# Kernel optimization log

Hardware: AMD Instinct MI355X
Metric: run time of the kernel (lower is better)

Reference implementation:

```python
import jax, jax.numpy as jnp
import numpy as np

N_NODES = 50000
N_EDGES = 800000
IN_DIM = 128
HID = 64
N_LAYERS = 4  # num_layers=5 in source -> 4 GINConv layers
BN_EPS = 1e-5


def setup_inputs() -> dict:
    key = jax.random.key(0)
    ks = jax.random.split(key, 16)
    h = jax.random.normal(ks[0], (N_NODES, IN_DIM), dtype=jnp.float32)
    src = jax.random.randint(ks[1], (N_EDGES,), 0, N_NODES, dtype=jnp.int32)
    dst = jax.random.randint(ks[2], (N_EDGES,), 0, N_NODES, dtype=jnp.int32)
    s = 0.05
    # layer 0 params (IN_DIM -> HID -> HID)
    W1_0 = jax.random.normal(ks[3], (IN_DIM, HID), dtype=jnp.float32) * s
    b1_0 = jnp.zeros((HID,), jnp.float32)
    W2_0 = jax.random.normal(ks[4], (HID, HID), dtype=jnp.float32) * s
    b2_0 = jnp.zeros((HID,), jnp.float32)
    g_0 = jnp.ones((HID,), jnp.float32)
    be_0 = jnp.zeros((HID,), jnp.float32)
    # layers 1..3 params stacked (HID -> HID -> HID)
    W1s = jax.random.normal(ks[5], (N_LAYERS - 1, HID, HID), dtype=jnp.float32) * s
    b1s = jnp.zeros((N_LAYERS - 1, HID), jnp.float32)
    W2s = jax.random.normal(ks[6], (N_LAYERS - 1, HID, HID), dtype=jnp.float32) * s
    b2s = jnp.zeros((N_LAYERS - 1, HID), jnp.float32)
    gs = jnp.ones((N_LAYERS - 1, HID), jnp.float32)
    bes = jnp.zeros((N_LAYERS - 1, HID), jnp.float32)
    return dict(h=h, src=src, dst=dst,
                W1_0=W1_0, b1_0=b1_0, W2_0=W2_0, b2_0=b2_0, g_0=g_0, be_0=be_0,
                W1s=W1s, b1s=b1s, W2s=W2s, b2s=b2s, gs=gs, bes=bes)


def _gin_layer(h, src, dst, W1, b1, W2, b2, gamma, beta):
    # GINConv (eps=0, sum aggregation): z = h + sum_{j->i} h_j
    agg = jax.ops.segment_sum(h[src], dst, num_segments=N_NODES)  # [N, d]
    z = h + agg
    # MLP: Linear -> ReLU -> Linear
    z = jax.nn.relu(z @ W1 + b1) @ W2 + b2
    # BatchNorm1d (training mode: batch statistics over nodes)
    mean = jnp.mean(z, axis=0)
    var = jnp.var(z, axis=0)
    z = (z - mean) * jax.lax.rsqrt(var + BN_EPS) * gamma + beta
    return jax.nn.relu(z)


def reference(h, src, dst, W1_0, b1_0, W2_0, b2_0, g_0, be_0,
              W1s, b1s, W2s, b2s, gs, bes):
    h = _gin_layer(h, src, dst, W1_0, b1_0, W2_0, b2_0, g_0, be_0)
    for i in range(N_LAYERS - 1):
        h = _gin_layer(h, src, dst, W1s[i], b1s[i], W2s[i], b2s[i], gs[i], bes[i])
    return h
```

## Files before the change

kernel.cpp:

```cpp
#include <hip/hip_runtime.h>
#include <hip/hip_bf16.h>

static constexpr int NN = 50000;
static constexpr int NE = 800000;
static constexpr float BN_EPS = 1e-5f;

static constexpr int NB  = 128;
static constexpr int NPB = 391;
static constexpr int CAP = 8192;
static constexpr int CHUNK = 2048;
static constexpr int SRNG = 12500;

__device__ __forceinline__ float bflo(unsigned u) { return __uint_as_float(u << 16); }
__device__ __forceinline__ float bfhi(unsigned u) { return __uint_as_float(u & 0xffff0000u); }
__device__ __forceinline__ unsigned short f2bf(float f) {
    unsigned u = __float_as_uint(f);
    unsigned r = (u + 0x7fffu + ((u >> 16) & 1u)) >> 16;
    return (unsigned short)r;
}

__global__ __launch_bounds__(256) void zero_kernel(int* __restrict__ ptr, int n)
{
    int i = blockIdx.x * 256 + threadIdx.x;
    if (i < n) ptr[i] = 0;
}

__global__ __launch_bounds__(256) void binA_kernel(
    const int* __restrict__ src, const int* __restrict__ dst,
    int* __restrict__ gcount, unsigned* __restrict__ tmp)
{
    __shared__ unsigned stage[CHUNK];
    __shared__ int hist[NB], base[NB], gpos[NB];

    const int t = threadIdx.x;
    const int cb = blockIdx.x * CHUNK;
    const int total = min(CHUNK, NE - cb);

    if (t < NB) hist[t] = 0;
    __syncthreads();

    int mb[8], mslot[8];
    unsigned mv[8];
    #pragma unroll
    for (int k = 0; k < 8; ++k) {
        int e = cb + k * 256 + t;
        mb[k] = -1;
        if (e < NE) {
            int s = src[e];
            int d = dst[e];
            int b = d / NPB;
            mb[k] = b;
            mv[k] = ((unsigned)d << 16) | (unsigned)s;
            mslot[k] = atomicAdd(&hist[b], 1);
        }
    }
    __syncthreads();

    if (t < NB) base[t] = hist[t];
    __syncthreads();
    for (int ofs = 1; ofs < NB; ofs <<= 1) {
        int v = (t >= ofs && t < NB) ? base[t - ofs] : 0;
        __syncthreads();
        if (t < NB) base[t] += v;
        __syncthreads();
    }
    if (t < NB && hist[t] > 0)
        gpos[t] = t * CAP + atomicAdd(&gcount[t], hist[t]);
    __syncthreads();

    #pragma unroll
    for (int k = 0; k < 8; ++k) {
        if (mb[k] >= 0) {
            int b = mb[k];
            stage[(base[b] - hist[b]) + mslot[k]] = mv[k];
        }
    }
    __syncthreads();

    for (int i = t; i < total; i += 256) {
        unsigned v = stage[i];
        int b = (int)(v >> 16) / NPB;
        int pos = gpos[b] + (i - (base[b] - hist[b]));
        tmp[pos] = v;
    }
}

__global__ __launch_bounds__(256) void binB_kernel(
    const unsigned* __restrict__ tmp, const int* __restrict__ gcount,
    int* __restrict__ off, int* __restrict__ eidx)
{
    __shared__ int gb[NB];
    __shared__ int hist4[NPB * 4];
    __shared__ int hs[512];
    __shared__ int cur4[NPB * 4];
    __shared__ int base_s;

    const int t = threadIdx.x;
    const int b = blockIdx.x;
    const int n0 = b * NPB;
    const int n1 = min(n0 + NPB, NN);
    const int nnodes = n1 - n0;
    const int cnt = gcount[b];

    if (t < NB) gb[t] = gcount[t];
    for (int i = t; i < NPB * 4; i += 256) hist4[i] = 0;
    __syncthreads();
    for (int ofs = 1; ofs < NB; ofs <<= 1) {
        int v = (t >= ofs && t < NB) ? gb[t - ofs] : 0;
        __syncthreads();
        if (t < NB) gb[t] += v;
        __syncthreads();
    }
    if (t == 0) base_s = (b == 0) ? 0 : gb[b - 1];
    __syncthreads();
    const int base = base_s;

    const unsigned* tb = tmp + (size_t)b * CAP;
    for (int i = t; i < cnt; i += 256) {
        unsigned v = tb[i];
        int d = (int)(v >> 16);
        int s = (int)(v & 0xffffu);
        atomicAdd(&hist4[(d - n0) * 4 + s / SRNG], 1);
    }
    __syncthreads();
    {
        int n = t;
        hs[t] = (n < NPB) ? (hist4[n * 4] + hist4[n * 4 + 1] +
                             hist4[n * 4 + 2] + hist4[n * 4 + 3]) : 0;
        n = t + 256;
        hs[t + 256] = (n < NPB) ? (hist4[n * 4] + hist4[n * 4 + 1] +
                                   hist4[n * 4 + 2] + hist4[n * 4 + 3]) : 0;
    }
    __syncthreads();
    for (int ofs = 1; ofs < 512; ofs <<= 1) {
        int a0 = (t >= ofs) ? hs[t - ofs] : 0;
        int a1 = hs[t + 256 - ofs];
        __syncthreads();
        hs[t] += a0;
        hs[t + 256] += a1;
        __syncthreads();
    }
    for (int n = t; n < nnodes; n += 256) {
        int h0 = hist4[n * 4], h1 = hist4[n * 4 + 1], h2 = hist4[n * 4 + 2];
        int tot = h0 + h1 + h2 + hist4[n * 4 + 3];
        int c = base + hs[n] - tot;
        off[n0 + n] = c;
        cur4[n * 4 + 0] = c; c += h0;
        cur4[n * 4 + 1] = c; c += h1;
        cur4[n * 4 + 2] = c; c += h2;
        cur4[n * 4 + 3] = c;
    }
    if (b == NB - 1 && t == 0) off[NN] = base + cnt;
    __syncthreads();
    for (int i = t; i < cnt; i += 256) {
        unsigned v = tb[i];
        int d = (int)(v >> 16);
        int s = (int)(v & 0xffffu);
        int pos = atomicAdd(&cur4[(d - n0) * 4 + s / SRNG], 1);
        eidx[pos] = s;
    }
}

template<int D, bool NORM>
__global__ __launch_bounds__(256) void proj_kernel(
    const void* __restrict__ hin_, const float* __restrict__ W1,
    const float* __restrict__ gsum, const float* __restrict__ gsq,
    const float* __restrict__ gamma, const float* __restrict__ beta,
    unsigned short* __restrict__ p)
{
    constexpr int RPB = 128;
    __shared__ float XsT[64][132];
    __shared__ float Ws[64][64];
    __shared__ float scs[64], shs[64];

    const int t = threadIdx.x;
    const int rowbase = blockIdx.x * RPB;

    if (NORM) {
        if (t < 64) {
            const float invn = 1.f / (float)NN;
            float mean = gsum[t] * invn;
            float var  = gsq[t] * invn - mean * mean;
            float sc   = gamma[t] * rsqrtf(var + BN_EPS);
            scs[t] = sc;
            shs[t] = beta[t] - mean * sc;
        }
        __syncthreads();
    }

    const int tc = t & 7;
    const int tr = t >> 3;
    const int c0 = tc * 8;
    const int r0 = tr * 4;

    float acc[4][8];
    #pragma unroll
    for (int i = 0; i < 4; ++i)
        #pragma unroll
        for (int j = 0; j < 8; ++j) acc[i][j] = 0.f;

    for (int kc = 0; kc < D; kc += 64) {
        if (kc) __syncthreads();
        {
            const float4* wg = reinterpret_cast<const float4*>(W1 + (size_t)kc * 64);
            float4* wl = reinterpret_cast<float4*>(&Ws[0][0]);
            for (int i = t; i < 64 * 16; i += 256) wl[i] = wg[i];
        }
        if constexpr (NORM) {
            const uint4* hb = reinterpret_cast<const uint4*>(hin_);
            int rr = t & 31, q = t >> 5;
            for (int i = 0; i < RPB; i += 32) {
                int r = i + rr;
                int gr = rowbase + r;
                uint4 v = make_uint4(0u, 0u, 0u, 0u);
                if (gr < NN) v = hb[gr * 8 + q];
                int c = q * 8;
                float f0 = bflo(v.x), f1 = bfhi(v.x), f2 = bflo(v.y), f3 = bfhi(v.y);
                float f4 = bflo(v.z), f5 = bfhi(v.z), f6 = bflo(v.w), f7 = bfhi(v.w);
                XsT[c + 0][r] = fmaxf(f0 * scs[c + 0] + shs[c + 0], 0.f);
                XsT[c + 1][r] = fmaxf(f1 * scs[c + 1] + shs[c + 1], 0.f);
                XsT[c + 2][r] = fmaxf(f2 * scs[c + 2] + shs[c + 2], 0.f);
                XsT[c + 3][r] = fmaxf(f3 * scs[c + 3] + shs[c + 3], 0.f);
                XsT[c + 4][r] = fmaxf(f4 * scs[c + 4] + shs[c + 4], 0.f);
                XsT[c + 5][r] = fmaxf(f5 * scs[c + 5] + shs[c + 5], 0.f);
                XsT[c + 6][r] = fmaxf(f6 * scs[c + 6] + shs[c + 6], 0.f);
                XsT[c + 7][r] = fmaxf(f7 * scs[c + 7] + shs[c + 7], 0.f);
            }
        } else {
            const float* hin = reinterpret_cast<const float*>(hin_);
            int rr = t & 15, q = t >> 4;
            for (int i = 0; i < RPB; i += 16) {
                int r = i + rr;
                int gr = rowbase + r;
                float4 v = make_float4(0.f, 0.f, 0.f, 0.f);
                if (gr < NN)
                    v = reinterpret_cast<const float4*>(hin + (size_t)gr * D + kc)[q];
                XsT[q * 4 + 0][r] = v.x;
                XsT[q * 4 + 1][r] = v.y;
                XsT[q * 4 + 2][r] = v.z;
                XsT[q * 4 + 3][r] = v.w;
            }
        }
        __syncthreads();

        for (int k = 0; k < 64; ++k) {
            float4 xa = *reinterpret_cast<const float4*>(&XsT[k][r0]);
            float4 wa = *reinterpret_cast<const float4*>(&Ws[k][c0]);
            float4 wb = *reinterpret_cast<const float4*>(&Ws[k][c0 + 4]);
            float x[4] = { xa.x, xa.y, xa.z, xa.w };
            float w[8] = { wa.x, wa.y, wa.z, wa.w, wb.x, wb.y, wb.z, wb.w };
            #pragma unroll
            for (int i = 0; i < 4; ++i)
                #pragma unroll
                for (int j = 0; j < 8; ++j) acc[i][j] += x[i] * w[j];
        }
    }

    #pragma unroll
    for (int i = 0; i < 4; ++i) {
        int gr = rowbase + r0 + i;
        if (gr < NN) {
            uint4 u;
            u.x = (unsigned)f2bf(acc[i][0]) | ((unsigned)f2bf(acc[i][1]) << 16);
            u.y = (unsigned)f2bf(acc[i][2]) | ((unsigned)f2bf(acc[i][3]) << 16);
            u.z = (unsigned)f2bf(acc[i][4]) | ((unsigned)f2bf(acc[i][5]) << 16);
            u.w = (unsigned)f2bf(acc[i][6]) | ((unsigned)f2bf(acc[i][7]) << 16);
            *reinterpret_cast<uint4*>(p + (size_t)gr * 64 + c0) = u;
        }
    }
}

__global__ __launch_bounds__(256) void gather_kernel(
    const unsigned short* __restrict__ p, const int* __restrict__ off,
    const int* __restrict__ eidx, const float* __restrict__ b1,
    unsigned short* __restrict__ Y)
{
    int gid = blockIdx.x * 256 + threadIdx.x;
    if (gid >= NN * 8) return;
    int row = gid >> 3;
    int q = gid & 7;

    const uint4* pb = reinterpret_cast<const uint4*>(p);
    uint4 u = pb[row * 8 + q];
    float a0 = bflo(u.x), a1 = bfhi(u.x), a2 = bflo(u.y), a3 = bfhi(u.y);
    float a4 = bflo(u.z), a5 = bfhi(u.z), a6 = bflo(u.w), a7 = bfhi(u.w);

    int e = off[row];
    const int end = off[row + 1];
    for (; e + 4 <= end; e += 4) {
        int s0 = eidx[e + 0], s1 = eidx[e + 1];
        int s2 = eidx[e + 2], s3 = eidx[e + 3];
        uint4 v0 = pb[s0 * 8 + q];
        uint4 v1 = pb[s1 * 8 + q];
        uint4 v2 = pb[s2 * 8 + q];
        uint4 v3 = pb[s3 * 8 + q];
        a0 += (bflo(v0.x) + bflo(v1.x)) + (bflo(v2.x) + bflo(v3.x));
        a1 += (bfhi(v0.x) + bfhi(v1.x)) + (bfhi(v2.x) + bfhi(v3.x));
        a2 += (bflo(v0.y) + bflo(v1.y)) + (bflo(v2.y) + bflo(v3.y));
        a3 += (bfhi(v0.y) + bfhi(v1.y)) + (bfhi(v2.y) + bfhi(v3.y));
        a4 += (bflo(v0.z) + bflo(v1.z)) + (bflo(v2.z) + bflo(v3.z));
        a5 += (bfhi(v0.z) + bfhi(v1.z)) + (bfhi(v2.z) + bfhi(v3.z));
        a6 += (bflo(v0.w) + bflo(v1.w)) + (bflo(v2.w) + bflo(v3.w));
        a7 += (bfhi(v0.w) + bfhi(v1.w)) + (bfhi(v2.w) + bfhi(v3.w));
    }
    for (; e < end; ++e) {
        uint4 v = pb[eidx[e] * 8 + q];
        a0 += bflo(v.x); a1 += bfhi(v.x); a2 += bflo(v.y); a3 += bfhi(v.y);
        a4 += bflo(v.z); a5 += bfhi(v.z); a6 += bflo(v.w); a7 += bfhi(v.w);
    }

    float4 blo = reinterpret_cast<const float4*>(b1)[q * 2];
    float4 bhi = reinterpret_cast<const float4*>(b1)[q * 2 + 1];
    a0 = fmaxf(a0 + blo.x, 0.f); a1 = fmaxf(a1 + blo.y, 0.f);
    a2 = fmaxf(a2 + blo.z, 0.f); a3 = fmaxf(a3 + blo.w, 0.f);
    a4 = fmaxf(a4 + bhi.x, 0.f); a5 = fmaxf(a5 + bhi.y, 0.f);
    a6 = fmaxf(a6 + bhi.z, 0.f); a7 = fmaxf(a7 + bhi.w, 0.f);

    uint4 o;
    o.x = (unsigned)f2bf(a0) | ((unsigned)f2bf(a1) << 16);
    o.y = (unsigned)f2bf(a2) | ((unsigned)f2bf(a3) << 16);
    o.z = (unsigned)f2bf(a4) | ((unsigned)f2bf(a5) << 16);
    o.w = (unsigned)f2bf(a6) | ((unsigned)f2bf(a7) << 16);
    reinterpret_cast<uint4*>(Y)[row * 8 + q] = o;
}

__global__ __launch_bounds__(256) void mlp2_kernel(
    const unsigned short* __restrict__ Y, const float* __restrict__ W2,
    const float* __restrict__ b2, unsigned short* __restrict__ zb,
    float* __restrict__ gsum, float* __restrict__ gsq)
{
    constexpr int RPB = 128;
    __shared__ float XsT[64][132];
    __shared__ float Ws[64][64];
    __shared__ float b2s[64], lsum[64], lsq[64];

    const int t = threadIdx.x;
    const int rowbase = blockIdx.x * RPB;

    if (t < 64) { b2s[t] = b2[t]; lsum[t] = 0.f; lsq[t] = 0.f; }

    {
        const float4* wg = reinterpret_cast<const float4*>(W2);
        float4* wl = reinterpret_cast<float4*>(&Ws[0][0]);
        for (int i = t; i < 64 * 16; i += 256) wl[i] = wg[i];
    }
    {
        const uint4* yb = reinterpret_cast<const uint4*>(Y);
        int rr = t & 31, qq = t >> 5;
        for (int i = 0; i < RPB; i += 32) {
            int r = i + rr;
            int gr = rowbase + r;
            uint4 v = make_uint4(0u, 0u, 0u, 0u);
            if (gr < NN) v = yb[gr * 8 + qq];
            int c = qq * 8;
            XsT[c + 0][r] = bflo(v.x); XsT[c + 1][r] = bfhi(v.x);
            XsT[c + 2][r] = bflo(v.y); XsT[c + 3][r] = bfhi(v.y);
            XsT[c + 4][r] = bflo(v.z); XsT[c + 5][r] = bfhi(v.z);
            XsT[c + 6][r] = bflo(v.w); XsT[c + 7][r] = bfhi(v.w);
        }
    }
    __syncthreads();

    const int tc = t & 7;
    const int tr = t >> 3;
    const int c0 = tc * 8;
    const int r0 = tr * 4;

    float acc[4][8];
    #pragma unroll
    for (int i = 0; i < 4; ++i)
        #pragma unroll
        for (int j = 0; j < 8; ++j) acc[i][j] = 0.f;

    for (int k = 0; k < 64; ++k) {
        float4 xa = *reinterpret_cast<const float4*>(&XsT[k][r0]);
        float4 wa = *reinterpret_cast<const float4*>(&Ws[k][c0]);
        float4 wb = *reinterpret_cast<const float4*>(&Ws[k][c0 + 4]);
        float x[4] = { xa.x, xa.y, xa.z, xa.w };
        float w[8] = { wa.x, wa.y, wa.z, wa.w, wb.x, wb.y, wb.z, wb.w };
        #pragma unroll
        for (int i = 0; i < 4; ++i)
            #pragma unroll
            for (int j = 0; j < 8; ++j) acc[i][j] += x[i] * w[j];
    }

    float s[8], sq[8];
    #pragma unroll
    for (int j = 0; j < 8; ++j) { s[j] = 0.f; sq[j] = 0.f; }

    #pragma unroll
    for (int i = 0; i < 4; ++i) {
        int gr = rowbase + r0 + i;
        if (gr < NN) {
            float zv[8];
            #pragma unroll
            for (int j = 0; j < 8; ++j) {
                zv[j] = acc[i][j] + b2s[c0 + j];
                s[j] += zv[j];
                sq[j] += zv[j] * zv[j];
            }
            uint4 o;
            o.x = (unsigned)f2bf(zv[0]) | ((unsigned)f2bf(zv[1]) << 16);
            o.y = (unsigned)f2bf(zv[2]) | ((unsigned)f2bf(zv[3]) << 16);
            o.z = (unsigned)f2bf(zv[4]) | ((unsigned)f2bf(zv[5]) << 16);
            o.w = (unsigned)f2bf(zv[6]) | ((unsigned)f2bf(zv[7]) << 16);
            *reinterpret_cast<uint4*>(zb + (size_t)gr * 64 + c0) = o;
        }
    }

    #pragma unroll
    for (int j = 0; j < 8; ++j) {
        s[j]  += __shfl_xor(s[j], 8);
        s[j]  += __shfl_xor(s[j], 16);
        s[j]  += __shfl_xor(s[j], 32);
        sq[j] += __shfl_xor(sq[j], 8);
        sq[j] += __shfl_xor(sq[j], 16);
        sq[j] += __shfl_xor(sq[j], 32);
    }
    if ((t & 56) == 0) {
        #pragma unroll
        for (int j = 0; j < 8; ++j) {
            atomicAdd(&lsum[c0 + j], s[j]);
            atomicAdd(&lsq[c0 + j], sq[j]);
        }
    }
    __syncthreads();
    if (t < 64) {
        atomicAdd(&gsum[t], lsum[t]);
        atomicAdd(&gsq[t], lsq[t]);
    }
}

__global__ __launch_bounds__(256) void norm_kernel(
    const unsigned short* __restrict__ zb,
    const float* __restrict__ gsum, const float* __restrict__ gsq,
    const float* __restrict__ gamma, const float* __restrict__ beta,
    float* __restrict__ out)
{
    __shared__ float sc[64], sh[64];
    int t = threadIdx.x;
    if (t < 64) {
        const float invn = 1.f / (float)NN;
        float mean = gsum[t] * invn;
        float var  = gsq[t] * invn - mean * mean;
        float s    = gamma[t] * rsqrtf(var + BN_EPS);
        sc[t] = s;
        sh[t] = beta[t] - mean * s;
    }
    __syncthreads();
    int idx = blockIdx.x * 256 + t;
    if (idx >= NN * 8) return;
    int row = idx >> 3;
    int q = idx & 7;
    int c = q * 8;
    uint4 v = reinterpret_cast<const uint4*>(zb)[idx];
    float f0 = bflo(v.x), f1 = bfhi(v.x), f2 = bflo(v.y), f3 = bfhi(v.y);
    float f4 = bflo(v.z), f5 = bfhi(v.z), f6 = bflo(v.w), f7 = bfhi(v.w);
    float4 lo, hi;
    lo.x = fmaxf(f0 * sc[c + 0] + sh[c + 0], 0.f);
    lo.y = fmaxf(f1 * sc[c + 1] + sh[c + 1], 0.f);
    lo.z = fmaxf(f2 * sc[c + 2] + sh[c + 2], 0.f);
    lo.w = fmaxf(f3 * sc[c + 3] + sh[c + 3], 0.f);
    hi.x = fmaxf(f4 * sc[c + 4] + sh[c + 4], 0.f);
    hi.y = fmaxf(f5 * sc[c + 5] + sh[c + 5], 0.f);
    hi.z = fmaxf(f6 * sc[c + 6] + sh[c + 6], 0.f);
    hi.w = fmaxf(f7 * sc[c + 7] + sh[c + 7], 0.f);
    float* o = out + (size_t)row * 64 + c;
    *reinterpret_cast<float4*>(o) = lo;
    *reinterpret_cast<float4*>(o + 4) = hi;
}

extern "C" void kernel_launch(void* const* d_in, const int* in_sizes, int n_in,
                              void* d_out, int out_size, void* d_ws, size_t ws_size,
                              hipStream_t stream)
{
    const float* h    = (const float*)d_in[0];
    const int*   src  = (const int*)d_in[1];
    const int*   dst  = (const int*)d_in[2];
    const float* W1_0 = (const float*)d_in[3];
    const float* b1_0 = (const float*)d_in[4];
    const float* W2_0 = (const float*)d_in[5];
    const float* b2_0 = (const float*)d_in[6];
    const float* g_0  = (const float*)d_in[7];
    const float* be_0 = (const float*)d_in[8];
    const float* W1st = (const float*)d_in[9];
    const float* b1st = (const float*)d_in[10];
    const float* W2st = (const float*)d_in[11];
    const float* b2st = (const float*)d_in[12];
    const float* gst  = (const float*)d_in[13];
    const float* best = (const float*)d_in[14];
    float* out = (float*)d_out;

    char* ws = (char*)d_ws;
    unsigned short* p  = (unsigned short*)ws;
    unsigned short* Y  = p + (size_t)NN * 64;
    unsigned short* zb = Y + (size_t)NN * 64;
    unsigned* tmp = (unsigned*)(zb + (size_t)NN * 64);
    int* eidx   = (int*)(tmp + (size_t)NB * CAP);
    float* stats = (float*)(eidx + NE);
    int* gcount = (int*)(stats + 512);
    int* off    = gcount + NB;

    zero_kernel<<<3, 256, 0, stream>>>((int*)stats, 512 + NB);
    binA_kernel<<<(NE + CHUNK - 1) / CHUNK, 256, 0, stream>>>(src, dst, gcount, tmp);
    binB_kernel<<<NB, 256, 0, stream>>>(tmp, gcount, off, eidx);

    const int gemmblk   = (NN + 127) / 128;
    const int gatherblk = (NN * 8 + 255) / 256;
    const int normblk   = (NN * 8 + 255) / 256;

    float* gs0 = stats + 0 * 128;
    proj_kernel<128, false><<<gemmblk, 256, 0, stream>>>(
        h, W1_0, nullptr, nullptr, nullptr, nullptr, p);
    gather_kernel<<<gatherblk, 256, 0, stream>>>(p, off, eidx, b1_0, Y);
    mlp2_kernel<<<gemmblk, 256, 0, stream>>>(Y, W2_0, b2_0, zb, gs0, gs0 + 64);

    const float* gammas[4] = { g_0, gst + 0, gst + 64, gst + 128 };
    const float* betas[4]  = { be_0, best + 0, best + 64, best + 128 };

    for (int l = 0; l < 3; ++l) {
        float* gsp = stats + l * 128;
        float* gsc = stats + (l + 1) * 128;
        proj_kernel<64, true><<<gemmblk, 256, 0, stream>>>(
            zb, W1st + l * 4096, gsp, gsp + 64, gammas[l], betas[l], p);
        gather_kernel<<<gatherblk, 256, 0, stream>>>(p, off, eidx, b1st + l * 64, Y);
        mlp2_kernel<<<gemmblk, 256, 0, stream>>>(
            Y, W2st + l * 4096, b2st + l * 64, zb, gsc, gsc + 64);
    }

    float* gs3 = stats + 3 * 128;
    norm_kernel<<<normblk, 256, 0, stream>>>(zb, gs3, gs3 + 64, gammas[3], betas[3], out);
}
```

Measured before the change: 247.8 us.

## Use bf16 MFMA for the 64-wide projection and second MLP GEMMs

```diff
diff --git a/kernel.cpp b/kernel.cpp
--- a/kernel.cpp
+++ b/kernel.cpp
@@ -10,6 +10,9 @@
 static constexpr int CAP = 8192;
 static constexpr int CHUNK = 2048;
 static constexpr int SRNG = 12500;
+
+typedef short bf16x8 __attribute__((ext_vector_type(8)));
+typedef float f32x4 __attribute__((ext_vector_type(4)));
 
 __device__ __forceinline__ float bflo(unsigned u) { return __uint_as_float(u << 16); }
 __device__ __forceinline__ float bfhi(unsigned u) { return __uint_as_float(u & 0xffff0000u); }
@@ -161,32 +164,17 @@
     }
 }
 
-template<int D, bool NORM>
-__global__ __launch_bounds__(256) void proj_kernel(
-    const void* __restrict__ hin_, const float* __restrict__ W1,
-    const float* __restrict__ gsum, const float* __restrict__ gsq,
-    const float* __restrict__ gamma, const float* __restrict__ beta,
+__global__ __launch_bounds__(256) void proj0_kernel(
+    const float* __restrict__ hin, const float* __restrict__ W1,
     unsigned short* __restrict__ p)
 {
+    constexpr int D = 128;
     constexpr int RPB = 128;
     __shared__ float XsT[64][132];
     __shared__ float Ws[64][64];
-    __shared__ float scs[64], shs[64];
 
     const int t = threadIdx.x;
     const int rowbase = blockIdx.x * RPB;
-
-    if (NORM) {
-        if (t < 64) {
-            const float invn = 1.f / (float)NN;
-            float mean = gsum[t] * invn;
-            float var  = gsq[t] * invn - mean * mean;
-            float sc   = gamma[t] * rsqrtf(var + BN_EPS);
-            scs[t] = sc;
-            shs[t] = beta[t] - mean * sc;
-        }
-        __syncthreads();
-    }
 
     const int tc = t & 7;
     const int tr = t >> 3;
@@ -206,28 +194,7 @@
             float4* wl = reinterpret_cast<float4*>(&Ws[0][0]);
             for (int i = t; i < 64 * 16; i += 256) wl[i] = wg[i];
         }
-        if constexpr (NORM) {
-            const uint4* hb = reinterpret_cast<const uint4*>(hin_);
-            int rr = t & 31, q = t >> 5;
-            for (int i = 0; i < RPB; i += 32) {
-                int r = i + rr;
-                int gr = rowbase + r;
-                uint4 v = make_uint4(0u, 0u, 0u, 0u);
-                if (gr < NN) v = hb[gr * 8 + q];
-                int c = q * 8;
-                float f0 = bflo(v.x), f1 = bfhi(v.x), f2 = bflo(v.y), f3 = bfhi(v.y);
-                float f4 = bflo(v.z), f5 = bfhi(v.z), f6 = bflo(v.w), f7 = bfhi(v.w);
-                XsT[c + 0][r] = fmaxf(f0 * scs[c + 0] + shs[c + 0], 0.f);
-                XsT[c + 1][r] = fmaxf(f1 * scs[c + 1] + shs[c + 1], 0.f);
-                XsT[c + 2][r] = fmaxf(f2 * scs[c + 2] + shs[c + 2], 0.f);
-                XsT[c + 3][r] = fmaxf(f3 * scs[c + 3] + shs[c + 3], 0.f);
-                XsT[c + 4][r] = fmaxf(f4 * scs[c + 4] + shs[c + 4], 0.f);
-                XsT[c + 5][r] = fmaxf(f5 * scs[c + 5] + shs[c + 5], 0.f);
-                XsT[c + 6][r] = fmaxf(f6 * scs[c + 6] + shs[c + 6], 0.f);
-                XsT[c + 7][r] = fmaxf(f7 * scs[c + 7] + shs[c + 7], 0.f);
-            }
-        } else {
-            const float* hin = reinterpret_cast<const float*>(hin_);
+        {
             int rr = t & 15, q = t >> 4;
             for (int i = 0; i < RPB; i += 16) {
                 int r = i + rr;
@@ -268,6 +235,147 @@
             *reinterpret_cast<uint4*>(p + (size_t)gr * 64 + c0) = u;
         }
     }
+}
+
+__global__ __launch_bounds__(256) void proj_mfma(
+    const unsigned short* __restrict__ zbin, const float* __restrict__ W1,
+    const float* __restrict__ gsum, const float* __restrict__ gsq,
+    const float* __restrict__ gamma, const float* __restrict__ beta,
+    unsigned short* __restrict__ p)
+{
+    __shared__ unsigned short Wt[64][72];
+    __shared__ float scs[64], shs[64];
+
+    const int t = threadIdx.x;
+    if (t < 64) {
+        const float invn = 1.f / (float)NN;
+        float mean = gsum[t] * invn;
+        float var  = gsq[t] * invn - mean * mean;
+        float sc   = gamma[t] * rsqrtf(var + BN_EPS);
+        scs[t] = sc;
+        shs[t] = beta[t] - mean * sc;
+    }
+    for (int i = t; i < 64 * 16; i += 256) {
+        int k = i >> 4, c0 = (i & 15) * 4;
+        float4 w = *reinterpret_cast<const float4*>(W1 + (size_t)k * 64 + c0);
+        Wt[c0 + 0][k] = f2bf(w.x); Wt[c0 + 1][k] = f2bf(w.y);
+        Wt[c0 + 2][k] = f2bf(w.z); Wt[c0 + 3][k] = f2bf(w.w);
+    }
+    __syncthreads();
+
+    const int wv = t >> 6;
+    const int l = t & 63;
+    const int g = l >> 4;
+    const int cl = l & 15;
+    const int rowbase = blockIdx.x * 64 + wv * 16;
+
+    int ar = min(rowbase + cl, NN - 1);
+    const unsigned short* yrow = zbin + (size_t)ar * 64;
+    bf16x8 a0, a1;
+    {
+        uint4 u0 = *reinterpret_cast<const uint4*>(yrow + 8 * g);
+        uint4 u1 = *reinterpret_cast<const uint4*>(yrow + 32 + 8 * g);
+        unsigned uu[8] = { u0.x, u0.y, u0.z, u0.w, u1.x, u1.y, u1.z, u1.w };
+        unsigned short oo[16];
+        #pragma unroll
+        for (int q = 0; q < 8; ++q) {
+            int kb = (q < 4) ? (8 * g + q * 2) : (32 + 8 * g + (q - 4) * 2);
+            float f0 = bflo(uu[q]), f1 = bfhi(uu[q]);
+            oo[q * 2 + 0] = f2bf(fmaxf(f0 * scs[kb + 0] + shs[kb + 0], 0.f));
+            oo[q * 2 + 1] = f2bf(fmaxf(f1 * scs[kb + 1] + shs[kb + 1], 0.f));
+        }
+        a0 = *reinterpret_cast<bf16x8*>(&oo[0]);
+        a1 = *reinterpret_cast<bf16x8*>(&oo[8]);
+    }
+
+    f32x4 acc[4];
+    #pragma unroll
+    for (int ct = 0; ct < 4; ++ct) acc[ct] = (f32x4){0.f, 0.f, 0.f, 0.f};
+
+    #pragma unroll
+    for (int ct = 0; ct < 4; ++ct) {
+        bf16x8 b0 = *reinterpret_cast<const bf16x8*>(&Wt[ct * 16 + cl][8 * g]);
+        bf16x8 b1 = *reinterpret_cast<const bf16x8*>(&Wt[ct * 16 + cl][32 + 8 * g]);
+        acc[ct] = __builtin_amdgcn_mfma_f32_16x16x32_bf16(a0, b0, acc[ct], 0, 0, 0);
+        acc[ct] = __builtin_amdgcn_mfma_f32_16x16x32_bf16(a1, b1, acc[ct], 0, 0, 0);
+    }
+
+    #pragma unroll
+    for (int ct = 0; ct < 4; ++ct) {
+        int col = ct * 16 + cl;
+        #pragma unroll
+        for (int j = 0; j < 4; ++j) {
+            int gr = rowbase + 4 * g + j;
+            if (gr < NN) p[(size_t)gr * 64 + col] = f2bf(acc[ct][j]);
+        }
+    }
+}
+
+__global__ __launch_bounds__(256) void mlp2_mfma(
+    const unsigned short* __restrict__ Y, const float* __restrict__ W2,
+    const float* __restrict__ b2, unsigned short* __restrict__ zb,
+    float* __restrict__ gsum, float* __restrict__ gsq)
+{
+    __shared__ unsigned short Wt[64][72];
+    __shared__ float b2s[64], lsum[64], lsq[64];
+
+    const int t = threadIdx.x;
+    if (t < 64) { b2s[t] = b2[t]; lsum[t] = 0.f; lsq[t] = 0.f; }
+    for (int i = t; i < 64 * 16; i += 256) {
+        int k = i >> 4, c0 = (i & 15) * 4;
+        float4 w = *reinterpret_cast<const float4*>(W2 + (size_t)k * 64 + c0);
+        Wt[c0 + 0][k] = f2bf(w.x); Wt[c0 + 1][k] = f2bf(w.y);
+        Wt[c0 + 2][k] = f2bf(w.z); Wt[c0 + 3][k] = f2bf(w.w);
+    }
+    __syncthreads();
+
+    const int wv = t >> 6;
+    const int l = t & 63;
+    const int g = l >> 4;
+    const int cl = l & 15;
+    const int rowbase = blockIdx.x * 64 + wv * 16;
+
+    int ar = min(rowbase + cl, NN - 1);
+    const unsigned short* yrow = Y + (size_t)ar * 64;
+    bf16x8 a0 = *reinterpret_cast<const bf16x8*>(yrow + 8 * g);
+    bf16x8 a1 = *reinterpret_cast<const bf16x8*>(yrow + 32 + 8 * g);
+
+    f32x4 acc[4];
+    #pragma unroll
+    for (int ct = 0; ct < 4; ++ct) acc[ct] = (f32x4){0.f, 0.f, 0.f, 0.f};
+
+    #pragma unroll
+    for (int ct = 0; ct < 4; ++ct) {
+        bf16x8 b0 = *reinterpret_cast<const bf16x8*>(&Wt[ct * 16 + cl][8 * g]);
+        bf16x8 b1 = *reinterpret_cast<const bf16x8*>(&Wt[ct * 16 + cl][32 + 8 * g]);
+        acc[ct] = __builtin_amdgcn_mfma_f32_16x16x32_bf16(a0, b0, acc[ct], 0, 0, 0);
+        acc[ct] = __builtin_amdgcn_mfma_f32_16x16x32_bf16(a1, b1, acc[ct], 0, 0, 0);
+    }
+
+    #pragma unroll
+    for (int ct = 0; ct < 4; ++ct) {
+        int col = ct * 16 + cl;
+        float bb = b2s[col];
+        float s = 0.f, sq = 0.f;
+        float zv[4];
+        #pragma unroll
+        for (int j = 0; j < 4; ++j) {
+            int gr = rowbase + 4 * g + j;
+            float z = acc[ct][j] + bb;
+            zv[j] = z;
+            if (gr < NN) { s += z; sq += z * z; }
+        }
+        s  += __shfl_xor(s, 16);  s  += __shfl_xor(s, 32);
+        sq += __shfl_xor(sq, 16); sq += __shfl_xor(sq, 32);
+        if (l < 16) { atomicAdd(&lsum[col], s); atomicAdd(&lsq[col], sq); }
+        #pragma unroll
+        for (int j = 0; j < 4; ++j) {
+            int gr = rowbase + 4 * g + j;
+            if (gr < NN) zb[(size_t)gr * 64 + col] = f2bf(zv[j]);
+        }
+    }
+    __syncthreads();
+    if (t < 64) { atomicAdd(&gsum[t], lsum[t]); atomicAdd(&gsq[t], lsq[t]); }
 }
 
 __global__ __launch_bounds__(256) void gather_kernel(
@@ -322,113 +430,6 @@
     o.z = (unsigned)f2bf(a4) | ((unsigned)f2bf(a5) << 16);
     o.w = (unsigned)f2bf(a6) | ((unsigned)f2bf(a7) << 16);
     reinterpret_cast<uint4*>(Y)[row * 8 + q] = o;
-}
-
-__global__ __launch_bounds__(256) void mlp2_kernel(
-    const unsigned short* __restrict__ Y, const float* __restrict__ W2,
-    const float* __restrict__ b2, unsigned short* __restrict__ zb,
-    float* __restrict__ gsum, float* __restrict__ gsq)
-{
-    constexpr int RPB = 128;
-    __shared__ float XsT[64][132];
-    __shared__ float Ws[64][64];
-    __shared__ float b2s[64], lsum[64], lsq[64];
-
-    const int t = threadIdx.x;
-    const int rowbase = blockIdx.x * RPB;
-
-    if (t < 64) { b2s[t] = b2[t]; lsum[t] = 0.f; lsq[t] = 0.f; }
-
-    {
-        const float4* wg = reinterpret_cast<const float4*>(W2);
-        float4* wl = reinterpret_cast<float4*>(&Ws[0][0]);
-        for (int i = t; i < 64 * 16; i += 256) wl[i] = wg[i];
-    }
-    {
-        const uint4* yb = reinterpret_cast<const uint4*>(Y);
-        int rr = t & 31, qq = t >> 5;
-        for (int i = 0; i < RPB; i += 32) {
-            int r = i + rr;
-            int gr = rowbase + r;
-            uint4 v = make_uint4(0u, 0u, 0u, 0u);
-            if (gr < NN) v = yb[gr * 8 + qq];
-            int c = qq * 8;
-            XsT[c + 0][r] = bflo(v.x); XsT[c + 1][r] = bfhi(v.x);
-            XsT[c + 2][r] = bflo(v.y); XsT[c + 3][r] = bfhi(v.y);
-            XsT[c + 4][r] = bflo(v.z); XsT[c + 5][r] = bfhi(v.z);
-            XsT[c + 6][r] = bflo(v.w); XsT[c + 7][r] = bfhi(v.w);
-        }
-    }
-    __syncthreads();
-
-    const int tc = t & 7;
-    const int tr = t >> 3;
-    const int c0 = tc * 8;
-    const int r0 = tr * 4;
-
-    float acc[4][8];
-    #pragma unroll
-    for (int i = 0; i < 4; ++i)
-        #pragma unroll
-        for (int j = 0; j < 8; ++j) acc[i][j] = 0.f;
-
-    for (int k = 0; k < 64; ++k) {
-        float4 xa = *reinterpret_cast<const float4*>(&XsT[k][r0]);
-        float4 wa = *reinterpret_cast<const float4*>(&Ws[k][c0]);
-        float4 wb = *reinterpret_cast<const float4*>(&Ws[k][c0 + 4]);
-        float x[4] = { xa.x, xa.y, xa.z, xa.w };
-        float w[8] = { wa.x, wa.y, wa.z, wa.w, wb.x, wb.y, wb.z, wb.w };
-        #pragma unroll
-        for (int i = 0; i < 4; ++i)
-            #pragma unroll
-            for (int j = 0; j < 8; ++j) acc[i][j] += x[i] * w[j];
-    }
-
-    float s[8], sq[8];
-    #pragma unroll
-    for (int j = 0; j < 8; ++j) { s[j] = 0.f; sq[j] = 0.f; }
-
-    #pragma unroll
-    for (int i = 0; i < 4; ++i) {
-        int gr = rowbase + r0 + i;
-        if (gr < NN) {
-            float zv[8];
-            #pragma unroll
-            for (int j = 0; j < 8; ++j) {
-                zv[j] = acc[i][j] + b2s[c0 + j];
-                s[j] += zv[j];
-                sq[j] += zv[j] * zv[j];
-            }
-            uint4 o;
-            o.x = (unsigned)f2bf(zv[0]) | ((unsigned)f2bf(zv[1]) << 16);
-            o.y = (unsigned)f2bf(zv[2]) | ((unsigned)f2bf(zv[3]) << 16);
-            o.z = (unsigned)f2bf(zv[4]) | ((unsigned)f2bf(zv[5]) << 16);
-            o.w = (unsigned)f2bf(zv[6]) | ((unsigned)f2bf(zv[7]) << 16);
-            *reinterpret_cast<uint4*>(zb + (size_t)gr * 64 + c0) = o;
-        }
-    }
-
-    #pragma unroll
-    for (int j = 0; j < 8; ++j) {
-        s[j]  += __shfl_xor(s[j], 8);
-        s[j]  += __shfl_xor(s[j], 16);
-        s[j]  += __shfl_xor(s[j], 32);
-        sq[j] += __shfl_xor(sq[j], 8);
-        sq[j] += __shfl_xor(sq[j], 16);
-        sq[j] += __shfl_xor(sq[j], 32);
-    }
-    if ((t & 56) == 0) {
-        #pragma unroll
-        for (int j = 0; j < 8; ++j) {
-            atomicAdd(&lsum[c0 + j], s[j]);
-            atomicAdd(&lsq[c0 + j], sq[j]);
-        }
-    }
-    __syncthreads();
-    if (t < 64) {
-        atomicAdd(&gsum[t], lsum[t]);
-        atomicAdd(&gsq[t], lsq[t]);
-    }
 }
 
 __global__ __launch_bounds__(256) void norm_kernel(
@@ -506,14 +507,14 @@
     binB_kernel<<<NB, 256, 0, stream>>>(tmp, gcount, off, eidx);
 
     const int gemmblk   = (NN + 127) / 128;
+    const int mfmablk   = (NN + 63) / 64;
     const int gatherblk = (NN * 8 + 255) / 256;
     const int normblk   = (NN * 8 + 255) / 256;
 
     float* gs0 = stats + 0 * 128;
-    proj_kernel<128, false><<<gemmblk, 256, 0, stream>>>(
-        h, W1_0, nullptr, nullptr, nullptr, nullptr, p);
+    proj0_kernel<<<gemmblk, 256, 0, stream>>>(h, W1_0, p);
     gather_kernel<<<gatherblk, 256, 0, stream>>>(p, off, eidx, b1_0, Y);
-    mlp2_kernel<<<gemmblk, 256, 0, stream>>>(Y, W2_0, b2_0, zb, gs0, gs0 + 64);
+    mlp2_mfma<<<mfmablk, 256, 0, stream>>>(Y, W2_0, b2_0, zb, gs0, gs0 + 64);
 
     const float* gammas[4] = { g_0, gst + 0, gst + 64, gst + 128 };
     const float* betas[4]  = { be_0, best + 0, best + 64, best + 128 };
@@ -521,10 +522,10 @@
     for (int l = 0; l < 3; ++l) {
         float* gsp = stats + l * 128;
         float* gsc = stats + (l + 1) * 128;
-        proj_kernel<64, true><<<gemmblk, 256, 0, stream>>>(
+        proj_mfma<<<mfmablk, 256, 0, stream>>>(
             zb, W1st + l * 4096, gsp, gsp + 64, gammas[l], betas[l], p);
         gather_kernel<<<gatherblk, 256, 0, stream>>>(p, off, eidx, b1st + l * 64, Y);
-        mlp2_kernel<<<gemmblk, 256, 0, stream>>>(
+        mlp2_mfma<<<mfmablk, 256, 0, stream>>>(
             Y, W2st + l * 4096, b2st + l * 64, zb, gsc, gsc + 64);
     }
 
```

Measured after the change: 252.9 us. 1.02x slower.

## Use bf16 MFMA for first-layer projection and unroll gather by eight

Applied to the files above, without the earlier changes.

```diff
diff --git a/kernel.cpp b/kernel.cpp
--- a/kernel.cpp
+++ b/kernel.cpp
@@ -10,6 +10,9 @@
 static constexpr int CAP = 8192;
 static constexpr int CHUNK = 2048;
 static constexpr int SRNG = 12500;
+
+typedef short bf16x8 __attribute__((ext_vector_type(8)));
+typedef float f32x4 __attribute__((ext_vector_type(4)));
 
 __device__ __forceinline__ float bflo(unsigned u) { return __uint_as_float(u << 16); }
 __device__ __forceinline__ float bfhi(unsigned u) { return __uint_as_float(u & 0xffff0000u); }
@@ -161,9 +164,67 @@
     }
 }
 
-template<int D, bool NORM>
+__global__ __launch_bounds__(256) void proj0_mfma(
+    const float* __restrict__ hin, const float* __restrict__ W1,
+    unsigned short* __restrict__ p)
+{
+    __shared__ unsigned short Wt[64][136];
+
+    const int t = threadIdx.x;
+    for (int i = t; i < 128 * 16; i += 256) {
+        int k = i >> 4, c0 = (i & 15) * 4;
+        float4 w = *reinterpret_cast<const float4*>(W1 + (size_t)k * 64 + c0);
+        Wt[c0 + 0][k] = f2bf(w.x); Wt[c0 + 1][k] = f2bf(w.y);
+        Wt[c0 + 2][k] = f2bf(w.z); Wt[c0 + 3][k] = f2bf(w.w);
+    }
+    __syncthreads();
+
+    const int wv = t >> 6;
+    const int l = t & 63;
+    const int g = l >> 4;
+    const int cl = l & 15;
+    const int rowbase = blockIdx.x * 64 + wv * 16;
+
+    int ar = min(rowbase + cl, NN - 1);
+    const float* hrow = hin + (size_t)ar * 128;
+    bf16x8 a[4];
+    #pragma unroll
+    for (int kk = 0; kk < 4; ++kk) {
+        float4 f0 = *reinterpret_cast<const float4*>(hrow + kk * 32 + 8 * g);
+        float4 f1 = *reinterpret_cast<const float4*>(hrow + kk * 32 + 8 * g + 4);
+        unsigned short oo[8] = { f2bf(f0.x), f2bf(f0.y), f2bf(f0.z), f2bf(f0.w),
+                                 f2bf(f1.x), f2bf(f1.y), f2bf(f1.z), f2bf(f1.w) };
+        a[kk] = *reinterpret_cast<bf16x8*>(oo);
+    }
+
+    f32x4 acc[4];
+    #pragma unroll
+    for (int ct = 0; ct < 4; ++ct) acc[ct] = (f32x4){0.f, 0.f, 0.f, 0.f};
+
+    #pragma unroll
+    for (int ct = 0; ct < 4; ++ct) {
+        #pragma unroll
+        for (int kk = 0; kk < 4; ++kk) {
+            bf16x8 w = *reinterpret_cast<const bf16x8*>(
+                &Wt[ct * 16 + cl][kk * 32 + 8 * g]);
+            acc[ct] = __builtin_amdgcn_mfma_f32_16x16x32_bf16(w, a[kk], acc[ct], 0, 0, 0);
+        }
+    }
+
+    int gr = rowbase + cl;
+    if (gr < NN) {
+        #pragma unroll
+        for (int ct = 0; ct < 4; ++ct) {
+            unsigned lo = (unsigned)f2bf(acc[ct][0]) | ((unsigned)f2bf(acc[ct][1]) << 16);
+            unsigned hi = (unsigned)f2bf(acc[ct][2]) | ((unsigned)f2bf(acc[ct][3]) << 16);
+            *reinterpret_cast<uint2*>(p + (size_t)gr * 64 + ct * 16 + 4 * g) =
+                make_uint2(lo, hi);
+        }
+    }
+}
+
 __global__ __launch_bounds__(256) void proj_kernel(
-    const void* __restrict__ hin_, const float* __restrict__ W1,
+    const unsigned short* __restrict__ zbin, const float* __restrict__ W1,
     const float* __restrict__ gsum, const float* __restrict__ gsq,
     const float* __restrict__ gamma, const float* __restrict__ beta,
     unsigned short* __restrict__ p)
@@ -176,17 +237,15 @@
     const int t = threadIdx.x;
     const int rowbase = blockIdx.x * RPB;
 
-    if (NORM) {
-        if (t < 64) {
-            const float invn = 1.f / (float)NN;
-            float mean = gsum[t] * invn;
-            float var  = gsq[t] * invn - mean * mean;
-            float sc   = gamma[t] * rsqrtf(var + BN_EPS);
-            scs[t] = sc;
-            shs[t] = beta[t] - mean * sc;
-        }
-        __syncthreads();
-    }
+    if (t < 64) {
+        const float invn = 1.f / (float)NN;
+        float mean = gsum[t] * invn;
+        float var  = gsq[t] * invn - mean * mean;
+        float sc   = gamma[t] * rsqrtf(var + BN_EPS);
+        scs[t] = sc;
+        shs[t] = beta[t] - mean * sc;
+    }
+    __syncthreads();
 
     const int tc = t & 7;
     const int tr = t >> 3;
@@ -199,61 +258,44 @@
         #pragma unroll
         for (int j = 0; j < 8; ++j) acc[i][j] = 0.f;
 
-    for (int kc = 0; kc < D; kc += 64) {
-        if (kc) __syncthreads();
-        {
-            const float4* wg = reinterpret_cast<const float4*>(W1 + (size_t)kc * 64);
-            float4* wl = reinterpret_cast<float4*>(&Ws[0][0]);
-            for (int i = t; i < 64 * 16; i += 256) wl[i] = wg[i];
-        }
-        if constexpr (NORM) {
-            const uint4* hb = reinterpret_cast<const uint4*>(hin_);
-            int rr = t & 31, q = t >> 5;
-            for (int i = 0; i < RPB; i += 32) {
-                int r = i + rr;
-                int gr = rowbase + r;
-                uint4 v = make_uint4(0u, 0u, 0u, 0u);
-                if (gr < NN) v = hb[gr * 8 + q];
-                int c = q * 8;
-                float f0 = bflo(v.x), f1 = bfhi(v.x), f2 = bflo(v.y), f3 = bfhi(v.y);
-                float f4 = bflo(v.z), f5 = bfhi(v.z), f6 = bflo(v.w), f7 = bfhi(v.w);
-                XsT[c + 0][r] = fmaxf(f0 * scs[c + 0] + shs[c + 0], 0.f);
-                XsT[c + 1][r] = fmaxf(f1 * scs[c + 1] + shs[c + 1], 0.f);
-                XsT[c + 2][r] = fmaxf(f2 * scs[c + 2] + shs[c + 2], 0.f);
-                XsT[c + 3][r] = fmaxf(f3 * scs[c + 3] + shs[c + 3], 0.f);
-                XsT[c + 4][r] = fmaxf(f4 * scs[c + 4] + shs[c + 4], 0.f);
-                XsT[c + 5][r] = fmaxf(f5 * scs[c + 5] + shs[c + 5], 0.f);
-                XsT[c + 6][r] = fmaxf(f6 * scs[c + 6] + shs[c + 6], 0.f);
-                XsT[c + 7][r] = fmaxf(f7 * scs[c + 7] + shs[c + 7], 0.f);
-            }
-        } else {
-            const float* hin = reinterpret_cast<const float*>(hin_);
-            int rr = t & 15, q = t >> 4;
-            for (int i = 0; i < RPB; i += 16) {
-                int r = i + rr;
-                int gr = rowbase + r;
-                float4 v = make_float4(0.f, 0.f, 0.f, 0.f);
-                if (gr < NN)
-                    v = reinterpret_cast<const float4*>(hin + (size_t)gr * D + kc)[q];
-                XsT[q * 4 + 0][r] = v.x;
-                XsT[q * 4 + 1][r] = v.y;
-                XsT[q * 4 + 2][r] = v.z;
-                XsT[q * 4 + 3][r] = v.w;
-            }
-        }
-        __syncthreads();
-
-        for (int k = 0; k < 64; ++k) {
-            float4 xa = *reinterpret_cast<const float4*>(&XsT[k][r0]);
-            float4 wa = *reinterpret_cast<const float4*>(&Ws[k][c0]);
-            float4 wb = *reinterpret_cast<const float4*>(&Ws[k][c0 + 4]);
-            float x[4] = { xa.x, xa.y, xa.z, xa.w };
-            float w[8] = { wa.x, wa.y, wa.z, wa.w, wb.x, wb.y, wb.z, wb.w };
+    {
+        const float4* wg = reinterpret_cast<const float4*>(W1);
+        float4* wl = reinterpret_cast<float4*>(&Ws[0][0]);
+        for (int i = t; i < 64 * 16; i += 256) wl[i] = wg[i];
+    }
+    {
+        const uint4* hb = reinterpret_cast<const uint4*>(zbin);
+        int rr = t & 31, q = t >> 5;
+        for (int i = 0; i < RPB; i += 32) {
+            int r = i + rr;
+            int gr = rowbase + r;
+            uint4 v = make_uint4(0u, 0u, 0u, 0u);
+            if (gr < NN) v = hb[gr * 8 + q];
+            int c = q * 8;
+            float f0 = bflo(v.x), f1 = bfhi(v.x), f2 = bflo(v.y), f3 = bfhi(v.y);
+            float f4 = bflo(v.z), f5 = bfhi(v.z), f6 = bflo(v.w), f7 = bfhi(v.w);
+            XsT[c + 0][r] = fmaxf(f0 * scs[c + 0] + shs[c + 0], 0.f);
+            XsT[c + 1][r] = fmaxf(f1 * scs[c + 1] + shs[c + 1], 0.f);
+            XsT[c + 2][r] = fmaxf(f2 * scs[c + 2] + shs[c + 2], 0.f);
+            XsT[c + 3][r] = fmaxf(f3 * scs[c + 3] + shs[c + 3], 0.f);
+            XsT[c + 4][r] = fmaxf(f4 * scs[c + 4] + shs[c + 4], 0.f);
+            XsT[c + 5][r] = fmaxf(f5 * scs[c + 5] + shs[c + 5], 0.f);
+            XsT[c + 6][r] = fmaxf(f6 * scs[c + 6] + shs[c + 6], 0.f);
+            XsT[c + 7][r] = fmaxf(f7 * scs[c + 7] + shs[c + 7], 0.f);
+        }
+    }
+    __syncthreads();
+
+    for (int k = 0; k < 64; ++k) {
+        float4 xa = *reinterpret_cast<const float4*>(&XsT[k][r0]);
+        float4 wa = *reinterpret_cast<const float4*>(&Ws[k][c0]);
+        float4 wb = *reinterpret_cast<const float4*>(&Ws[k][c0 + 4]);
+        float x[4] = { xa.x, xa.y, xa.z, xa.w };
+        float w[8] = { wa.x, wa.y, wa.z, wa.w, wb.x, wb.y, wb.z, wb.w };
+        #pragma unroll
+        for (int i = 0; i < 4; ++i)
             #pragma unroll
-            for (int i = 0; i < 4; ++i)
-                #pragma unroll
-                for (int j = 0; j < 8; ++j) acc[i][j] += x[i] * w[j];
-        }
+            for (int j = 0; j < 8; ++j) acc[i][j] += x[i] * w[j];
     }
 
     #pragma unroll
@@ -287,6 +329,21 @@
 
     int e = off[row];
     const int end = off[row + 1];
+    for (; e + 8 <= end; e += 8) {
+        int si[8];
+        #pragma unroll
+        for (int k = 0; k < 8; ++k) si[k] = eidx[e + k];
+        uint4 vv[8];
+        #pragma unroll
+        for (int k = 0; k < 8; ++k) vv[k] = pb[si[k] * 8 + q];
+        #pragma unroll
+        for (int k = 0; k < 8; ++k) {
+            a0 += bflo(vv[k].x); a1 += bfhi(vv[k].x);
+            a2 += bflo(vv[k].y); a3 += bfhi(vv[k].y);
+            a4 += bflo(vv[k].z); a5 += bfhi(vv[k].z);
+            a6 += bflo(vv[k].w); a7 += bfhi(vv[k].w);
+        }
+    }
     for (; e + 4 <= end; e += 4) {
         int s0 = eidx[e + 0], s1 = eidx[e + 1];
         int s2 = eidx[e + 2], s3 = eidx[e + 3];
@@ -506,12 +563,12 @@
     binB_kernel<<<NB, 256, 0, stream>>>(tmp, gcount, off, eidx);
 
     const int gemmblk   = (NN + 127) / 128;
+    const int mfmablk   = (NN + 63) / 64;
     const int gatherblk = (NN * 8 + 255) / 256;
     const int normblk   = (NN * 8 + 255) / 256;
 
     float* gs0 = stats + 0 * 128;
-    proj_kernel<128, false><<<gemmblk, 256, 0, stream>>>(
-        h, W1_0, nullptr, nullptr, nullptr, nullptr, p);
+    proj0_mfma<<<mfmablk, 256, 0, stream>>>(h, W1_0, p);
     gather_kernel<<<gatherblk, 256, 0, stream>>>(p, off, eidx, b1_0, Y);
     mlp2_kernel<<<gemmblk, 256, 0, stream>>>(Y, W2_0, b2_0, zb, gs0, gs0 + 64);
 
@@ -521,7 +578,7 @@
     for (int l = 0; l < 3; ++l) {
         float* gsp = stats + l * 128;
         float* gsc = stats + (l + 1) * 128;
-        proj_kernel<64, true><<<gemmblk, 256, 0, stream>>>(
+        proj_kernel<<<gemmblk, 256, 0, stream>>>(
             zb, W1st + l * 4096, gsp, gsp + 64, gammas[l], betas[l], p);
         gather_kernel<<<gatherblk, 256, 0, stream>>>(p, off, eidx, b1st + l * 64, Y);
         mlp2_kernel<<<gemmblk, 256, 0, stream>>>(
```

New measurement: 251.2 us. No clear change (+1.4%).
